# Kernel tuning notes

Measured on AMD Instinct MI355X. Metric: run time of the kernel, lower is better.

## Reference

```python
import jax, jax.numpy as jnp
import numpy as np

N, F, H, C, K = 4096, 128, 128, 10, 4  # nodes, feat dim, hidden, classes, num_graphs
EDGE_P = 0.005


def setup_inputs() -> dict:
    key = jax.random.key(0)
    ks = jax.random.split(key, 20)
    feat_matrix = jax.random.normal(ks[0], (N, F), jnp.float32)
    # binary adjacency (dense_to_sparse + GCNConv without edge_weight => weights all 1)
    adj = (jax.random.uniform(ks[1], (N, N, K)) < EDGE_P).astype(jnp.float32)
    adj_matrix = adj * (1.0 - jnp.eye(N, dtype=jnp.float32))[:, :, None]  # no self loops in input
    s = 0.05
    gcn_w1 = jax.random.normal(ks[2], (K, F, H), jnp.float32) * s
    gcn_b1 = jnp.zeros((K, H), jnp.float32)
    gcn_w2 = jax.random.normal(ks[3], (K, H, H), jnp.float32) * s
    gcn_b2 = jnp.zeros((K, H), jnp.float32)
    # PyTorch LSTM params (gate order i,f,g,o), forward and backward directions
    wih_f = jax.random.normal(ks[4], (4 * H, H), jnp.float32) * s
    whh_f = jax.random.normal(ks[5], (4 * H, H), jnp.float32) * s
    bih_f = jnp.zeros((4 * H,), jnp.float32)
    bhh_f = jnp.zeros((4 * H,), jnp.float32)
    wih_b = jax.random.normal(ks[6], (4 * H, H), jnp.float32) * s
    whh_b = jax.random.normal(ks[7], (4 * H, H), jnp.float32) * s
    bih_b = jnp.zeros((4 * H,), jnp.float32)
    bhh_b = jnp.zeros((4 * H,), jnp.float32)
    rnn_out_w = jax.random.normal(ks[8], (1, 2 * H), jnp.float32) * s
    rnn_out_b = jnp.zeros((1,), jnp.float32)
    out_w = jax.random.normal(ks[9], (C, H), jnp.float32) * s
    out_b = jnp.zeros((C,), jnp.float32)
    get_item_index = jnp.arange(N, dtype=jnp.int64)
    set_index = jax.random.randint(ks[10], (1024,), 0, N).astype(jnp.int64)
    val_index = jax.random.randint(ks[11], (1024,), 0, N).astype(jnp.int64)
    mask_matrix = jnp.ones((N,), jnp.bool_)
    return dict(feat_matrix=feat_matrix, adj_matrix=adj_matrix,
                gcn_w1=gcn_w1, gcn_b1=gcn_b1, gcn_w2=gcn_w2, gcn_b2=gcn_b2,
                wih_f=wih_f, whh_f=whh_f, bih_f=bih_f, bhh_f=bhh_f,
                wih_b=wih_b, whh_b=whh_b, bih_b=bih_b, bhh_b=bhh_b,
                rnn_out_w=rnn_out_w, rnn_out_b=rnn_out_b, out_w=out_w, out_b=out_b,
                get_item_index=get_item_index, set_index=set_index,
                val_index=val_index, mask_matrix=mask_matrix)


def _gcn_norm(adj):
    # GCNConv default: A_hat = A + I, sym-normalized D^-1/2 A_hat D^-1/2
    a_hat = adj + jnp.eye(adj.shape[0], dtype=adj.dtype)
    dinv = jax.lax.rsqrt(a_hat.sum(axis=1))
    return dinv[:, None] * a_hat * dinv[None, :]


def _lstm_dir(xs, wih, whh, bih, bhh, reverse):
    # xs: [N, K, H] -> hs: [N, K, H]; scan over the (short) block axis K
    n, h = xs.shape[0], whh.shape[1]
    def step(carry, x_t):
        hp, cp = carry
        g = x_t @ wih.T + hp @ whh.T + (bih + bhh)
        i, f, gg, o = jnp.split(g, 4, axis=-1)
        c = jax.nn.sigmoid(f) * cp + jax.nn.sigmoid(i) * jnp.tanh(gg)
        hn = jax.nn.sigmoid(o) * jnp.tanh(c)
        return (hn, c), hn
    init = (jnp.zeros((n, h), xs.dtype), jnp.zeros((n, h), xs.dtype))
    _, hs = jax.lax.scan(step, init, jnp.swapaxes(xs, 0, 1), reverse=reverse)
    return jnp.swapaxes(hs, 0, 1)


def reference(feat_matrix, adj_matrix, gcn_w1, gcn_b1, gcn_w2, gcn_b2,
              wih_f, whh_f, bih_f, bhh_f, wih_b, whh_b, bih_b, bhh_b,
              rnn_out_w, rnn_out_b, out_w, out_b,
              get_item_index, set_index, val_index, mask_matrix):
    k_blocks = adj_matrix.shape[-1]
    gnn_output = []
    for k in range(k_blocks):  # fixed small number of structurally distinct graph blocks
        an = _gcn_norm(adj_matrix[:, :, k])                 # [N, N]
        h = an @ (feat_matrix @ gcn_w1[k]) + gcn_b1[k]      # GCNConv 1 (no activation)
        h = an @ (h @ gcn_w2[k]) + gcn_b2[k]                # GCNConv 2
        gnn_output.append(h)
    gnn_out = jnp.stack(gnn_output, axis=1)                 # [N, K, H]
    h_fwd = _lstm_dir(gnn_out, wih_f, whh_f, bih_f, bhh_f, reverse=False)
    h_bwd = _lstm_dir(gnn_out, wih_b, whh_b, bih_b, bhh_b, reverse=True)
    rnn_hid = jnp.concatenate([h_fwd, h_bwd], axis=-1)      # [N, K, 2H]
    attn = jax.nn.softmax(rnn_hid @ rnn_out_w.T + rnn_out_b, axis=1)  # [N, K, 1]
    pooled = (gnn_out * attn).sum(axis=1)                   # [N, H]
    return jax.nn.softmax(pooled @ out_w.T + out_b, axis=-1)  # [N, C]
```

## Files before the change

### kernel.cpp

```cpp
#include <hip/hip_runtime.h>
#include <hip/hip_bf16.h>

#define NN 4096
#define HD 128
#define KG 4
#define NC 10
#define CAP 64

typedef __attribute__((ext_vector_type(8))) short bf16x8;
typedef __attribute__((ext_vector_type(4))) float f32x4;

__device__ inline unsigned short f2b(float x) {
    unsigned u = __float_as_uint(x);
    return (unsigned short)((u + 0x7FFFu + ((u >> 16) & 1u)) >> 16);
}
__device__ inline float b2f(unsigned short b) {
    return __uint_as_float((unsigned)b << 16);
}

__global__ __launch_bounds__(256) void setup_kernel(
    const float* __restrict__ adj, const float* __restrict__ feat,
    const float* __restrict__ wih_f, const float* __restrict__ whh_f,
    const float* __restrict__ bih_f, const float* __restrict__ bhh_f,
    const float* __restrict__ wih_b, const float* __restrict__ whh_b,
    const float* __restrict__ bih_b, const float* __restrict__ bhh_b,
    const float* __restrict__ gw1, const float* __restrict__ gw2,
    float* __restrict__ dinv, int* __restrict__ ecnt,
    unsigned short* __restrict__ edges, unsigned* __restrict__ featb,
    unsigned short* __restrict__ Wp, float* __restrict__ bp,
    unsigned short* __restrict__ Wg1p, unsigned short* __restrict__ Wg2p)
{
    int b = blockIdx.x;
    __shared__ int cnt[KG];
    if (b < NN) {
        int i = b;
        if (threadIdx.x < KG) cnt[threadIdx.x] = 0;
        __syncthreads();
        const float4* row = (const float4*)(adj + (size_t)i * NN * KG);
        for (int j = threadIdx.x; j < NN; j += 256) {
            float4 v = row[j];
            if (v.x != 0.f) { int p = atomicAdd(&cnt[0], 1); if (p < CAP) edges[((size_t)(0 * NN + i)) * CAP + p] = (unsigned short)j; }
            if (v.y != 0.f) { int p = atomicAdd(&cnt[1], 1); if (p < CAP) edges[((size_t)(1 * NN + i)) * CAP + p] = (unsigned short)j; }
            if (v.z != 0.f) { int p = atomicAdd(&cnt[2], 1); if (p < CAP) edges[((size_t)(2 * NN + i)) * CAP + p] = (unsigned short)j; }
            if (v.w != 0.f) { int p = atomicAdd(&cnt[3], 1); if (p < CAP) edges[((size_t)(3 * NN + i)) * CAP + p] = (unsigned short)j; }
        }
        __syncthreads();
        if (threadIdx.x < KG) {
            int c = cnt[threadIdx.x];
            ecnt[threadIdx.x * NN + i] = c > CAP ? CAP : c;
            dinv[threadIdx.x * NN + i] = rsqrtf((float)c + 1.0f);
        }
    } else if (b < NN + 1024) {
        int t = (b - NN) * 256 + threadIdx.x;
        int dir = t >> 17, rem = t & 131071;
        int n = rem >> 8, k = rem & 255;
        int hq = n >> 6, g = (n >> 4) & 3, hr = n & 15;
        int row = g * HD + hq * 16 + hr;
        const float* wih = dir ? wih_b : wih_f;
        const float* whh = dir ? whh_b : whh_f;
        Wp[t] = f2b(k < HD ? wih[row * HD + k] : whh[row * HD + (k - HD)]);
    } else if (b < NN + 1280) {
        int t = (b - NN - 1024) * 256 + threadIdx.x;
        int n = t >> 7, k = t & 127;
        Wg1p[t] = f2b(gw1[(((size_t)(n >> 7)) * HD + k) * HD + (n & 127)]);
    } else if (b < NN + 1536) {
        int t = (b - NN - 1280) * 256 + threadIdx.x;
        int n = t >> 7, k = t & 127;
        Wg2p[t] = f2b(gw2[(((size_t)(n >> 7)) * HD + k) * HD + (n & 127)]);
    } else if (b < NN + 2560) {
        int t = (b - NN - 1536) * 256 + threadIdx.x;
        float2 v = *(const float2*)&feat[2 * (size_t)t];
        featb[t] = (unsigned)f2b(v.x) | ((unsigned)f2b(v.y) << 16);
    } else {
        int t = (b - NN - 2560) * 256 + threadIdx.x;
        if (t < 1024) {
            int dir = t >> 9, n = t & 511;
            int hq = n >> 6, g = (n >> 4) & 3, hr = n & 15;
            int row = g * HD + hq * 16 + hr;
            bp[t] = dir ? (bih_b[row] + bhh_b[row]) : (bih_f[row] + bhh_f[row]);
        }
    }
}

__global__ __launch_bounds__(256) void gemm_gcn_mfma(
    const unsigned short* __restrict__ Ab, int a_per_k,
    const unsigned short* __restrict__ Bp, float* __restrict__ C)
{
    __shared__ unsigned short Abuf[64 * 40];
    __shared__ unsigned short Bbuf[128 * 40];
    int kg = blockIdx.x, m0 = blockIdx.y * 64;
    const unsigned short* A = Ab + (a_per_k ? (size_t)kg * NN * HD : 0);
    int wid = threadIdx.x >> 6, lane = threadIdx.x & 63;
    int wm = wid >> 1, wn = wid & 1;
    int la = lane & 15, kb = (lane >> 4) * 8;
    f32x4 acc[2][4] = {};
    for (int ch = 0; ch < 4; ++ch) {
        {
            int t = threadIdx.x, r = t >> 2, q = t & 3;
            *(uint4*)&Abuf[r * 40 + q * 8] =
                *(const uint4*)&A[((size_t)(m0 + r)) * HD + ch * 32 + q * 8];
        }
#pragma unroll
        for (int it = 0; it < 2; ++it) {
            int f = threadIdx.x + it * 256;
            int r = f >> 2, q = f & 3;
            *(uint4*)&Bbuf[r * 40 + q * 8] =
                *(const uint4*)&Bp[((size_t)(kg * 128 + r)) * HD + ch * 32 + q * 8];
        }
        __syncthreads();
        bf16x8 a[2], bb[4];
#pragma unroll
        for (int m = 0; m < 2; ++m)
            a[m] = *(const bf16x8*)&Abuf[(wm * 32 + m * 16 + la) * 40 + kb];
#pragma unroll
        for (int n = 0; n < 4; ++n)
            bb[n] = *(const bf16x8*)&Bbuf[(wn * 64 + n * 16 + la) * 40 + kb];
#pragma unroll
        for (int m = 0; m < 2; ++m)
#pragma unroll
            for (int n = 0; n < 4; ++n)
                acc[m][n] = __builtin_amdgcn_mfma_f32_16x16x32_bf16(a[m], bb[n], acc[m][n], 0, 0, 0);
        __syncthreads();
    }
    float* Cb = C + (size_t)kg * NN * HD;
    int lj = lane >> 4;
#pragma unroll
    for (int m = 0; m < 2; ++m)
#pragma unroll
        for (int n = 0; n < 4; ++n)
#pragma unroll
            for (int j = 0; j < 4; ++j) {
                int r = m0 + wm * 32 + m * 16 + lj * 4 + j;
                int col = wn * 64 + n * 16 + la;
                Cb[(size_t)r * HD + col] = acc[m][n][j];
            }
}

template <int WF32>
__global__ __launch_bounds__(256) void spmm_kernel(
    const float* __restrict__ Z, const float* __restrict__ dinv,
    const int* __restrict__ ecnt, const unsigned short* __restrict__ edges,
    const float* __restrict__ bias, float* __restrict__ Out,
    unsigned* __restrict__ Outb)
{
    int wid = threadIdx.x >> 6;
    int lane = threadIdx.x & 63;
    int idx = blockIdx.x * 4 + wid;
    int k = idx >> 12;
    int i = idx & (NN - 1);
    int cnt = ecnt[idx];
    float di = dinv[idx];
    const unsigned short* el = edges + (size_t)idx * CAP;
    const float* Zk = Z + (size_t)k * NN * HD;
    int h2 = lane * 2;
    float ax = 0.f, ay = 0.f;
    for (int e = 0; e < cnt; ++e) {
        int j = el[e];
        float dj = dinv[(k << 12) + j];
        float2 z = *(const float2*)(Zk + (size_t)j * HD + h2);
        ax = fmaf(dj, z.x, ax);
        ay = fmaf(dj, z.y, ay);
    }
    float2 zi = *(const float2*)(Zk + (size_t)i * HD + h2);
    ax = fmaf(di, zi.x, ax);
    ay = fmaf(di, zi.y, ay);
    float2 bv = *(const float2*)(bias + k * HD + h2);
    float2 o;
    o.x = fmaf(di, ax, bv.x);
    o.y = fmaf(di, ay, bv.y);
    if (WF32) *(float2*)(Out + (size_t)idx * HD + h2) = o;
    Outb[(size_t)idx * 64 + lane] = (unsigned)f2b(o.x) | ((unsigned)f2b(o.y) << 16);
}

__global__ __launch_bounds__(256) void lstm_fused(
    const unsigned short* __restrict__ G2b, unsigned short* __restrict__ hsb,
    const unsigned short* __restrict__ Wp, const float* __restrict__ bp)
{
    __shared__ unsigned short Bbuf[512 * 40];
    __shared__ unsigned short Abuf[64 * 40];
    __shared__ unsigned short hlds[64 * 136];
    int m0 = blockIdx.x * 64;
    int dir = blockIdx.y;
    int wid = threadIdx.x >> 6, lane = threadIdx.x & 63;
    int la = lane & 15, lj = lane >> 4, kb = lj * 8;
    const unsigned short* B = Wp + (size_t)dir * 512 * 256;
    float c_st[4][2][4] = {};
    float bias[2][4];
#pragma unroll
    for (int ch = 0; ch < 2; ++ch)
#pragma unroll
        for (int g = 0; g < 4; ++g)
            bias[ch][g] = bp[dir * 512 + wid * 128 + (ch * 4 + g) * 16 + la];

    for (int t = 0; t < KG; ++t) {
        int kin = dir ? (KG - 1 - t) : t;
        f32x4 acc[4][8] = {};
        int nch = (t == 0) ? 4 : 8;
        for (int ch = 0; ch < nch; ++ch) {
            if (ch < 4) {
                int r = threadIdx.x >> 2, q = threadIdx.x & 3;
                *(uint4*)&Abuf[r * 40 + q * 8] =
                    *(const uint4*)&G2b[((size_t)kin * NN + m0 + r) * HD + ch * 32 + q * 8];
            }
#pragma unroll
            for (int it = 0; it < 8; ++it) {
                int f = threadIdx.x + it * 256;
                int r = f >> 2, q = f & 3;
                *(uint4*)&Bbuf[r * 40 + q * 8] =
                    *(const uint4*)&B[(size_t)r * 256 + ch * 32 + q * 8];
            }
            __syncthreads();
            bf16x8 bfr[8];
#pragma unroll
            for (int fi = 0; fi < 8; ++fi)
                bfr[fi] = *(const bf16x8*)&Bbuf[(wid * 128 + fi * 16 + la) * 40 + kb];
#pragma unroll
            for (int m = 0; m < 4; ++m) {
                bf16x8 afr = (ch < 4)
                    ? *(const bf16x8*)&Abuf[(m * 16 + la) * 40 + kb]
                    : *(const bf16x8*)&hlds[(m * 16 + la) * 136 + (ch - 4) * 32 + kb];
#pragma unroll
                for (int fi = 0; fi < 8; ++fi)
                    acc[m][fi] = __builtin_amdgcn_mfma_f32_16x16x32_bf16(afr, bfr[fi], acc[m][fi], 0, 0, 0);
            }
            __syncthreads();
        }
        unsigned short* hout = hsb + ((size_t)(dir * KG + kin) * NN) * HD;
#pragma unroll
        for (int m = 0; m < 4; ++m)
#pragma unroll
            for (int j = 0; j < 4; ++j) {
                int r = m * 16 + lj * 4 + j;
#pragma unroll
                for (int chf = 0; chf < 2; ++chf) {
                    int h = wid * 32 + chf * 16 + la;
                    float gi = acc[m][chf * 4 + 0][j] + bias[chf][0];
                    float gf = acc[m][chf * 4 + 1][j] + bias[chf][1];
                    float gg = acc[m][chf * 4 + 2][j] + bias[chf][2];
                    float go = acc[m][chf * 4 + 3][j] + bias[chf][3];
                    float cold = c_st[m][chf][j];
                    float si = 1.f / (1.f + __expf(-gi));
                    float sf = 1.f / (1.f + __expf(-gf));
                    float so = 1.f / (1.f + __expf(-go));
                    float e2g = __expf(2.f * gg);
                    float tg = 1.f - 2.f / (e2g + 1.f);
                    float cn = fmaf(sf, cold, si * tg);
                    float e2c = __expf(2.f * cn);
                    float tc = 1.f - 2.f / (e2c + 1.f);
                    c_st[m][chf][j] = cn;
                    unsigned short hb = f2b(so * tc);
                    hlds[r * 136 + h] = hb;
                    hout[(size_t)(m0 + r) * HD + h] = hb;
                }
            }
        __syncthreads();
    }
}

__global__ __launch_bounds__(256) void finalize_kernel(
    const float* __restrict__ gnn, const unsigned* __restrict__ hsu,
    const float* __restrict__ rw, const float* __restrict__ ow,
    const float* __restrict__ ob, float* __restrict__ out)
{
    int wid = threadIdx.x >> 6, lane = threadIdx.x & 63;
    int n = blockIdx.x * 4 + wid;
    int u0 = 2 * lane;
    float w0 = rw[u0], w1 = rw[u0 + 1];
    float w2 = rw[HD + u0], w3 = rw[HD + u0 + 1];
    float lg[KG];
#pragma unroll
    for (int k = 0; k < KG; ++k) {
        unsigned hf = hsu[((size_t)k * NN + n) * 64 + lane];
        unsigned hb = hsu[((size_t)(KG + k) * NN + n) * 64 + lane];
        lg[k] = b2f((unsigned short)hf) * w0 + b2f((unsigned short)(hf >> 16)) * w1
              + b2f((unsigned short)hb) * w2 + b2f((unsigned short)(hb >> 16)) * w3;
    }
#pragma unroll
    for (int s = 32; s > 0; s >>= 1)
#pragma unroll
        for (int k = 0; k < KG; ++k) lg[k] += __shfl_xor(lg[k], s);
    float mx = lg[0];
#pragma unroll
    for (int k = 1; k < KG; ++k) mx = fmaxf(mx, lg[k]);
    float es[KG], se = 0.f;
#pragma unroll
    for (int k = 0; k < KG; ++k) { es[k] = __expf(lg[k] - mx); se += es[k]; }
    float inv = 1.f / se;
    float p0 = 0.f, p1 = 0.f;
#pragma unroll
    for (int k = 0; k < KG; ++k) {
        float a = es[k] * inv;
        float2 g = *(const float2*)(gnn + ((size_t)k * NN + n) * HD + u0);
        p0 = fmaf(a, g.x, p0);
        p1 = fmaf(a, g.y, p1);
    }
    float oc[NC];
#pragma unroll
    for (int c = 0; c < NC; ++c)
        oc[c] = p0 * ow[c * HD + u0] + p1 * ow[c * HD + u0 + 1];
#pragma unroll
    for (int s = 32; s > 0; s >>= 1)
#pragma unroll
        for (int c = 0; c < NC; ++c) oc[c] += __shfl_xor(oc[c], s);
    float omx = oc[0] + ob[0];
#pragma unroll
    for (int c = 0; c < NC; ++c) { oc[c] += ob[c]; omx = fmaxf(omx, oc[c]); }
    float osum = 0.f;
#pragma unroll
    for (int c = 0; c < NC; ++c) { oc[c] = __expf(oc[c] - omx); osum += oc[c]; }
    float oinv = 1.f / osum;
    if (lane < NC) out[(size_t)n * NC + lane] = oc[lane] * oinv;
}

extern "C" void kernel_launch(void* const* d_in, const int* in_sizes, int n_in,
                              void* d_out, int out_size, void* d_ws, size_t ws_size,
                              hipStream_t stream)
{
    const float* feat  = (const float*)d_in[0];
    const float* adj   = (const float*)d_in[1];
    const float* gw1   = (const float*)d_in[2];
    const float* gb1   = (const float*)d_in[3];
    const float* gw2   = (const float*)d_in[4];
    const float* gb2   = (const float*)d_in[5];
    const float* wih_f = (const float*)d_in[6];
    const float* whh_f = (const float*)d_in[7];
    const float* bih_f = (const float*)d_in[8];
    const float* bhh_f = (const float*)d_in[9];
    const float* wih_b = (const float*)d_in[10];
    const float* whh_b = (const float*)d_in[11];
    const float* bih_b = (const float*)d_in[12];
    const float* bhh_b = (const float*)d_in[13];
    const float* rw    = (const float*)d_in[14];
    const float* ow    = (const float*)d_in[16];
    const float* ob    = (const float*)d_in[17];
    float* out = (float*)d_out;

    char* ws = (char*)d_ws;
    float*          dinv  = (float*)(ws);
    int*            ecnt  = (int*)(ws + 65536);
    unsigned short* edges = (unsigned short*)(ws + 131072);
    unsigned*       featb = (unsigned*)(ws + 2228224);
    float*          Z     = (float*)(ws + 3276800);
    unsigned*       G1b   = (unsigned*)(ws + 11665408);
    float*          G2    = (float*)(ws + 15859712);
    unsigned*       G2b   = (unsigned*)(ws + 24248320);
    unsigned short* hsb   = (unsigned short*)(ws + 28442624);
    unsigned short* Wp    = (unsigned short*)(ws + 36831232);
    float*          bp    = (float*)(ws + 37355520);
    unsigned short* Wg1p  = (unsigned short*)(ws + 37359616);
    unsigned short* Wg2p  = (unsigned short*)(ws + 37490688);

    setup_kernel<<<NN + 2564, 256, 0, stream>>>(
        adj, feat, wih_f, whh_f, bih_f, bhh_f, wih_b, whh_b, bih_b, bhh_b,
        gw1, gw2, dinv, ecnt, edges, featb, Wp, bp, Wg1p, Wg2p);
    gemm_gcn_mfma<<<dim3(KG, 64), 256, 0, stream>>>((const unsigned short*)featb, 0, Wg1p, Z);
    spmm_kernel<0><<<KG * NN / 4, 256, 0, stream>>>(Z, dinv, ecnt, edges, gb1, nullptr, G1b);
    gemm_gcn_mfma<<<dim3(KG, 64), 256, 0, stream>>>((const unsigned short*)G1b, 1, Wg2p, Z);
    spmm_kernel<1><<<KG * NN / 4, 256, 0, stream>>>(Z, dinv, ecnt, edges, gb2, G2, G2b);
    lstm_fused<<<dim3(64, 2), 256, 0, stream>>>((const unsigned short*)G2b, hsb, Wp, bp);
    finalize_kernel<<<NN / 4, 256, 0, stream>>>(G2, (const unsigned*)hsb, rw, ow, ob, out);
}
```

Baseline: 544.2 us.

## Store GCN intermediates in bf16, prescale by dinv, ballot-aggregate edge compaction

Edge compaction in setup now uses a wavefront ballot and one LDS atomic per wave per graph instead of one atomic per nonzero. The GCN GEMM now folds the source-node dinv scaling into its epilogue and writes bf16 instead of fp32. The SpMM then gathers bf16 rows with edge indices broadcast by shuffle, unrolled by 4, and skips the per-edge dinv lookup. The fp32 copy of the final GCN output is dropped, and finalize reads the bf16 version. This cuts memory traffic and atomic contention, at the cost of bf16 rounding of the intermediates and the final pooled features.

```diff
diff --git a/kernel.cpp b/kernel.cpp
--- a/kernel.cpp
+++ b/kernel.cpp
@@ -34,15 +34,28 @@
     __shared__ int cnt[KG];
     if (b < NN) {
         int i = b;
+        int lane = threadIdx.x & 63;
         if (threadIdx.x < KG) cnt[threadIdx.x] = 0;
         __syncthreads();
         const float4* row = (const float4*)(adj + (size_t)i * NN * KG);
+        unsigned long long below = (1ull << lane) - 1ull;
         for (int j = threadIdx.x; j < NN; j += 256) {
             float4 v = row[j];
-            if (v.x != 0.f) { int p = atomicAdd(&cnt[0], 1); if (p < CAP) edges[((size_t)(0 * NN + i)) * CAP + p] = (unsigned short)j; }
-            if (v.y != 0.f) { int p = atomicAdd(&cnt[1], 1); if (p < CAP) edges[((size_t)(1 * NN + i)) * CAP + p] = (unsigned short)j; }
-            if (v.z != 0.f) { int p = atomicAdd(&cnt[2], 1); if (p < CAP) edges[((size_t)(2 * NN + i)) * CAP + p] = (unsigned short)j; }
-            if (v.w != 0.f) { int p = atomicAdd(&cnt[3], 1); if (p < CAP) edges[((size_t)(3 * NN + i)) * CAP + p] = (unsigned short)j; }
+#pragma unroll
+            for (int k = 0; k < KG; ++k) {
+                float comp = (k == 0) ? v.x : (k == 1) ? v.y : (k == 2) ? v.z : v.w;
+                unsigned long long mask = __ballot(comp != 0.f);
+                if (mask) {
+                    int base;
+                    if (lane == 0) base = atomicAdd(&cnt[k], __popcll(mask));
+                    base = __shfl(base, 0);
+                    if (comp != 0.f) {
+                        int p = base + (int)__popcll(mask & below);
+                        if (p < CAP)
+                            edges[((size_t)(k * NN + i)) * CAP + p] = (unsigned short)j;
+                    }
+                }
+            }
         }
         __syncthreads();
         if (threadIdx.x < KG) {
@@ -84,7 +97,8 @@
 
 __global__ __launch_bounds__(256) void gemm_gcn_mfma(
     const unsigned short* __restrict__ Ab, int a_per_k,
-    const unsigned short* __restrict__ Bp, float* __restrict__ C)
+    const unsigned short* __restrict__ Bp, const float* __restrict__ dinv,
+    unsigned short* __restrict__ Cb)
 {
     __shared__ unsigned short Abuf[64 * 40];
     __shared__ unsigned short Bbuf[128 * 40];
@@ -122,54 +136,58 @@
                 acc[m][n] = __builtin_amdgcn_mfma_f32_16x16x32_bf16(a[m], bb[n], acc[m][n], 0, 0, 0);
         __syncthreads();
     }
-    float* Cb = C + (size_t)kg * NN * HD;
+    unsigned short* Ck = Cb + (size_t)kg * NN * HD;
+    const float* dv = dinv + kg * NN;
     int lj = lane >> 4;
 #pragma unroll
     for (int m = 0; m < 2; ++m)
 #pragma unroll
-        for (int n = 0; n < 4; ++n)
-#pragma unroll
-            for (int j = 0; j < 4; ++j) {
-                int r = m0 + wm * 32 + m * 16 + lj * 4 + j;
+        for (int j = 0; j < 4; ++j) {
+            int r = m0 + wm * 32 + m * 16 + lj * 4 + j;
+            float d = dv[r];
+#pragma unroll
+            for (int n = 0; n < 4; ++n) {
                 int col = wn * 64 + n * 16 + la;
-                Cb[(size_t)r * HD + col] = acc[m][n][j];
-            }
-}
-
-template <int WF32>
+                Ck[(size_t)r * HD + col] = f2b(acc[m][n][j] * d);
+            }
+        }
+}
+
 __global__ __launch_bounds__(256) void spmm_kernel(
-    const float* __restrict__ Z, const float* __restrict__ dinv,
+    const unsigned* __restrict__ Zs, const float* __restrict__ dinv,
     const int* __restrict__ ecnt, const unsigned short* __restrict__ edges,
-    const float* __restrict__ bias, float* __restrict__ Out,
-    unsigned* __restrict__ Outb)
-{
-    int wid = threadIdx.x >> 6;
-    int lane = threadIdx.x & 63;
+    const float* __restrict__ bias, unsigned* __restrict__ Outb)
+{
+    int wid = threadIdx.x >> 6, lane = threadIdx.x & 63;
     int idx = blockIdx.x * 4 + wid;
-    int k = idx >> 12;
-    int i = idx & (NN - 1);
+    int k = idx >> 12, i = idx & (NN - 1);
     int cnt = ecnt[idx];
     float di = dinv[idx];
-    const unsigned short* el = edges + (size_t)idx * CAP;
-    const float* Zk = Z + (size_t)k * NN * HD;
-    int h2 = lane * 2;
+    const unsigned* Zk = Zs + (size_t)k * NN * 64;
+    int myj = edges[(size_t)idx * CAP + lane];
     float ax = 0.f, ay = 0.f;
-    for (int e = 0; e < cnt; ++e) {
-        int j = el[e];
-        float dj = dinv[(k << 12) + j];
-        float2 z = *(const float2*)(Zk + (size_t)j * HD + h2);
-        ax = fmaf(dj, z.x, ax);
-        ay = fmaf(dj, z.y, ay);
-    }
-    float2 zi = *(const float2*)(Zk + (size_t)i * HD + h2);
-    ax = fmaf(di, zi.x, ax);
-    ay = fmaf(di, zi.y, ay);
-    float2 bv = *(const float2*)(bias + k * HD + h2);
-    float2 o;
-    o.x = fmaf(di, ax, bv.x);
-    o.y = fmaf(di, ay, bv.y);
-    if (WF32) *(float2*)(Out + (size_t)idx * HD + h2) = o;
-    Outb[(size_t)idx * 64 + lane] = (unsigned)f2b(o.x) | ((unsigned)f2b(o.y) << 16);
+    for (int e = 0; e < cnt; e += 4) {
+        int rem = cnt - e;
+        int j0 = __shfl(myj, e);
+        int j1 = __shfl(myj, e + 1);
+        int j2 = __shfl(myj, e + 2);
+        int j3 = __shfl(myj, e + 3);
+        unsigned z0 = Zk[(size_t)j0 * 64 + lane];
+        unsigned z1 = (rem > 1) ? Zk[(size_t)j1 * 64 + lane] : 0u;
+        unsigned z2 = (rem > 2) ? Zk[(size_t)j2 * 64 + lane] : 0u;
+        unsigned z3 = (rem > 3) ? Zk[(size_t)j3 * 64 + lane] : 0u;
+        ax += (b2f((unsigned short)z0) + b2f((unsigned short)z1))
+            + (b2f((unsigned short)z2) + b2f((unsigned short)z3));
+        ay += (b2f((unsigned short)(z0 >> 16)) + b2f((unsigned short)(z1 >> 16)))
+            + (b2f((unsigned short)(z2 >> 16)) + b2f((unsigned short)(z3 >> 16)));
+    }
+    unsigned zi = Zk[(size_t)i * 64 + lane];
+    ax += b2f((unsigned short)zi);
+    ay += b2f((unsigned short)(zi >> 16));
+    float2 bv = *(const float2*)(bias + k * HD + 2 * lane);
+    float ox = fmaf(di, ax, bv.x);
+    float oy = fmaf(di, ay, bv.y);
+    Outb[(size_t)idx * 64 + lane] = (unsigned)f2b(ox) | ((unsigned)f2b(oy) << 16);
 }
 
 __global__ __launch_bounds__(256) void lstm_fused(
@@ -258,7 +276,7 @@
 }
 
 __global__ __launch_bounds__(256) void finalize_kernel(
-    const float* __restrict__ gnn, const unsigned* __restrict__ hsu,
+    const unsigned* __restrict__ gnnb, const unsigned* __restrict__ hsu,
     const float* __restrict__ rw, const float* __restrict__ ow,
     const float* __restrict__ ob, float* __restrict__ out)
 {
@@ -290,9 +308,9 @@
 #pragma unroll
     for (int k = 0; k < KG; ++k) {
         float a = es[k] * inv;
-        float2 g = *(const float2*)(gnn + ((size_t)k * NN + n) * HD + u0);
-        p0 = fmaf(a, g.x, p0);
-        p1 = fmaf(a, g.y, p1);
+        unsigned g = gnnb[((size_t)k * NN + n) * 64 + lane];
+        p0 = fmaf(a, b2f((unsigned short)g), p0);
+        p1 = fmaf(a, b2f((unsigned short)(g >> 16)), p1);
     }
     float oc[NC];
 #pragma unroll
@@ -340,23 +358,28 @@
     int*            ecnt  = (int*)(ws + 65536);
     unsigned short* edges = (unsigned short*)(ws + 131072);
     unsigned*       featb = (unsigned*)(ws + 2228224);
-    float*          Z     = (float*)(ws + 3276800);
-    unsigned*       G1b   = (unsigned*)(ws + 11665408);
-    float*          G2    = (float*)(ws + 15859712);
-    unsigned*       G2b   = (unsigned*)(ws + 24248320);
-    unsigned short* hsb   = (unsigned short*)(ws + 28442624);
-    unsigned short* Wp    = (unsigned short*)(ws + 36831232);
-    float*          bp    = (float*)(ws + 37355520);
-    unsigned short* Wg1p  = (unsigned short*)(ws + 37359616);
-    unsigned short* Wg2p  = (unsigned short*)(ws + 37490688);
+    unsigned short* Zs    = (unsigned short*)(ws + 3276800);
+    unsigned*       G1b   = (unsigned*)(ws + 7471104);
+    unsigned*       G2b   = (unsigned*)(ws + 11665408);
+    unsigned short* hsb   = (unsigned short*)(ws + 15859712);
+    unsigned short* Wp    = (unsigned short*)(ws + 24248320);
+    float*          bp    = (float*)(ws + 24772608);
+    unsigned short* Wg1p  = (unsigned short*)(ws + 24776704);
+    unsigned short* Wg2p  = (unsigned short*)(ws + 24907776);
 
     setup_kernel<<<NN + 2564, 256, 0, stream>>>(
         adj, feat, wih_f, whh_f, bih_f, bhh_f, wih_b, whh_b, bih_b, bhh_b,
         gw1, gw2, dinv, ecnt, edges, featb, Wp, bp, Wg1p, Wg2p);
-    gemm_gcn_mfma<<<dim3(KG, 64), 256, 0, stream>>>((const unsigned short*)featb, 0, Wg1p, Z);
-    spmm_kernel<0><<<KG * NN / 4, 256, 0, stream>>>(Z, dinv, ecnt, edges, gb1, nullptr, G1b);
-    gemm_gcn_mfma<<<dim3(KG, 64), 256, 0, stream>>>((const unsigned short*)G1b, 1, Wg2p, Z);
-    spmm_kernel<1><<<KG * NN / 4, 256, 0, stream>>>(Z, dinv, ecnt, edges, gb2, G2, G2b);
-    lstm_fused<<<dim3(64, 2), 256, 0, stream>>>((const unsigned short*)G2b, hsb, Wp, bp);
-    finalize_kernel<<<NN / 4, 256, 0, stream>>>(G2, (const unsigned*)hsb, rw, ow, ob, out);
-}
+    gemm_gcn_mfma<<<dim3(KG, 64), 256, 0, stream>>>(
+        (const unsigned short*)featb, 0, Wg1p, dinv, Zs);
+    spmm_kernel<<<KG * NN / 4, 256, 0, stream>>>(
+        (const unsigned*)Zs, dinv, ecnt, edges, gb1, G1b);
+    gemm_gcn_mfma<<<dim3(KG, 64), 256, 0, stream>>>(
+        (const unsigned short*)G1b, 1, Wg2p, dinv, Zs);
+    spmm_kernel<<<KG * NN / 4, 256, 0, stream>>>(
+        (const unsigned*)Zs, dinv, ecnt, edges, gb2, G2b);
+    lstm_fused<<<dim3(64, 2), 256, 0, stream>>>(
+        (const unsigned short*)G2b, hsb, Wp, bp);
+    finalize_kernel<<<NN / 4, 256, 0, stream>>>(
+        G2b, (const unsigned*)hsb, rw, ow, ob, out);
+}
```

New measurement: 499.3 us. -8.2%, faster.
